# Performance work log

Hardware: AMD Instinct MI355X
Metric: run time of the kernel (lower is better)

Reference implementation:

```python
import jax, jax.numpy as jnp
import numpy as np

D_IN = 2048
D_OUT = 2048
SEQ = 4096


def setup_inputs() -> dict:
    key = jax.random.key(0)
    kx, kq, kk, kv = jax.random.split(key, 4)
    x = jax.random.normal(kx, (SEQ, D_IN), dtype=jnp.float32)
    # torch.nn.Linear weights have shape [d_out, d_in]
    s = 1.0 / np.sqrt(D_IN)
    W_q = jax.random.uniform(kq, (D_OUT, D_IN), jnp.float32, -s, s)
    W_k = jax.random.uniform(kk, (D_OUT, D_IN), jnp.float32, -s, s)
    W_v = jax.random.uniform(kv, (D_OUT, D_IN), jnp.float32, -s, s)
    return {"x": x, "W_q": W_q, "W_k": W_k, "W_v": W_v}


def reference(x, W_q, W_k, W_v):
    # projections (torch Linear: x @ W.T)
    q = x @ W_q.T  # [S, D]
    k = x @ W_k.T
    v = x @ W_v.T
    scores = q @ k.T  # [S, S]
    scale = jnp.asarray(k.shape[-1], scores.dtype) ** 0.5
    attn = jax.nn.softmax(scores / scale, axis=-1)
    # post-softmax causal mask + row renormalization (faithful to source)
    S = scores.shape[0]
    mask = jnp.tril(jnp.ones((S, S), dtype=attn.dtype))
    masked = attn * mask
    masked = masked / masked.sum(axis=1, keepdims=True)
    return masked @ v  # [S, D]
```

## Files before the change

kernel.cpp:

```cpp
#include <hip/hip_runtime.h>
#include <hip/hip_bf16.h>
#include <math.h>


typedef __attribute__((ext_vector_type(8))) short bf16x8;
typedef __attribute__((ext_vector_type(4))) float f32x4;
typedef __attribute__((ext_vector_type(8))) unsigned short u16x8;
typedef __attribute__((ext_vector_type(4))) int iv4;

__device__ __forceinline__ unsigned short f2bf(float f) {
  unsigned int u = __float_as_uint(f);
  u += 0x7FFFu + ((u >> 16) & 1u);
  return (unsigned short)(u >> 16);
}

__device__ __forceinline__ void gload16(const unsigned short* g, unsigned short* l) {
  __builtin_amdgcn_global_load_lds(
      (const __attribute__((address_space(1))) void*)g,
      (__attribute__((address_space(3))) void*)l,
      16, 0, 0);
}

template <int OFF>
__device__ __forceinline__ bf16x8 dsr(unsigned addr) {
  iv4 r;
  asm volatile("ds_read_b128 %0, %1 offset:%2" : "=v"(r) : "v"(addr), "i"(OFF));
  return __builtin_bit_cast(bf16x8, r);
}

__global__ void cvt_f32_bf16(const float* __restrict__ in,
                             unsigned short* __restrict__ out, int n) {
  int i = (blockIdx.x * 256 + threadIdx.x) * 8;
  if (i >= n) return;
  float4 a = *(const float4*)(in + i);
  float4 b = *(const float4*)(in + i + 4);
  u16x8 r;
  r[0] = f2bf(a.x); r[1] = f2bf(a.y); r[2] = f2bf(a.z); r[3] = f2bf(a.w);
  r[4] = f2bf(b.x); r[5] = f2bf(b.y); r[6] = f2bf(b.z); r[7] = f2bf(b.w);
  *(u16x8*)(out + i) = r;
}

#define LGKM_SB()                                         \
  asm volatile("s_waitcnt lgkmcnt(0)" ::: "memory");      \
  __builtin_amdgcn_sched_barrier(0)

#define QMFMA(MB, NB, AF, BV)                                                 \
  _Pragma("unroll")                                                           \
  for (int _fm = 0; _fm < 4; ++_fm)                                           \
    _Pragma("unroll")                                                         \
    for (int _fn = 0; _fn < 2; ++_fn)                                         \
      _Pragma("unroll")                                                       \
      for (int _ks = 0; _ks < 2; ++_ks)                                       \
        acc[(MB) + _fm][(NB) + _fn] = __builtin_amdgcn_mfma_f32_16x16x32_bf16( \
            AF[_fm * 2 + _ks], BV[_fn * 2 + _ks], acc[(MB) + _fm][(NB) + _fn], \
            0, 0, 0);

#define STG_A(mhv, tau, bufv)                                                 \
  do {                                                                        \
    unsigned short* _d = lds + (bufv) * 32768 + (mhv) * 8192 + w * 512;       \
    gload16(pA + (size_t)((mhv) * 64) * KC + ((size_t)(tau) << 6), _d);       \
    gload16(pA + (size_t)(128 + (mhv) * 64) * KC + ((size_t)(tau) << 6),      \
            _d + 4096);                                                       \
  } while (0)

#define STG_B(nhv, tau, bufv)                                                 \
  do {                                                                        \
    unsigned short* _d = lds + (bufv) * 32768 + 16384 + (nhv) * 8192 + w * 512;\
    gload16(pB + (size_t)((nhv) * 32) * KC + ((size_t)(tau) << 6), _d);       \
    gload16(pB + (size_t)(128 + (nhv) * 32) * KC + ((size_t)(tau) << 6),      \
            _d + 4096);                                                       \
  } while (0)

#define VM_WAIT()                                                             \
  do {                                                                        \
    if (tail) { asm volatile("s_waitcnt vmcnt(0)" ::: "memory"); }            \
    else      { asm volatile("s_waitcnt vmcnt(8)" ::: "memory"); }            \
  } while (0)

template <int KC>
__device__ __forceinline__ void gemm_core(const unsigned short* __restrict__ Ab,
                                          const unsigned short* __restrict__ Bb,
                                          unsigned short* lds, int ktiles,
                                          f32x4 (&acc)[8][4]) {
  const int tid  = threadIdx.x;
  const int lane = tid & 63;
  const int w    = tid >> 6;
  const int wm   = w >> 2;
  const int wn   = w & 3;

  const int base  = w * 8 + (lane >> 3);
  const int gslot = (lane & 7) ^ ((lane >> 3) & 7);
  const unsigned short* pA = Ab + (size_t)base * KC + gslot * 8;
  const unsigned short* pB =
      Bb + (size_t)((base >> 5) * 64 + (base & 31)) * KC + gslot * 8;

  const unsigned lb = (unsigned)(size_t)&lds[0];
  const int rl = lane & 15, g = lane >> 4;
  const unsigned sw0 = (unsigned)(((0 + g) ^ (rl & 7)) * 16);
  const unsigned sw1 = (unsigned)(((4 + g) ^ (rl & 7)) * 16);
  const unsigned rA = lb + (unsigned)(wm * 8192 + rl * 128);
  const unsigned rB = lb + (unsigned)(wn * 4096 + rl * 128);

#pragma unroll
  for (int m = 0; m < 8; ++m)
#pragma unroll
    for (int n = 0; n < 4; ++n) acc[m][n] = f32x4{0.f, 0.f, 0.f, 0.f};

  STG_A(0, 0, 0); STG_B(0, 0, 0); STG_A(1, 0, 0); STG_B(1, 0, 0);
  if (ktiles > 1) {
    STG_A(0, 1, 1); STG_B(0, 1, 1); STG_A(1, 1, 1);
    asm volatile("s_waitcnt vmcnt(6)" ::: "memory");
  } else {
    asm volatile("s_waitcnt vmcnt(0)" ::: "memory");
  }
  __builtin_amdgcn_s_barrier();

  bf16x8 af0[8], af1[8], bv0[4], bv1[4];
  {
    const unsigned aA0 = rA + sw0, aA1 = rA + sw1;
    const unsigned aB0 = rB + sw0, aB1 = rB + sw1;
    af0[0] = dsr<0>(aA0);     af0[1] = dsr<0>(aA1);
    af0[2] = dsr<2048>(aA0);  af0[3] = dsr<2048>(aA1);
    af0[4] = dsr<4096>(aA0);  af0[5] = dsr<4096>(aA1);
    af0[6] = dsr<6144>(aA0);  af0[7] = dsr<6144>(aA1);
    bv0[0] = dsr<32768>(aB0); bv0[1] = dsr<32768>(aB1);
    bv0[2] = dsr<34816>(aB0); bv0[3] = dsr<34816>(aB1);
  }

  for (int t = 0; t < ktiles; ++t) {
    const unsigned bo  = (unsigned)(t & 1) << 16;
    const unsigned bon = (unsigned)((t + 1) & 1) << 16;
    const int buf = t & 1, nb = (t + 1) & 1;
    const bool s1 = (t + 1) < ktiles, s2 = (t + 2) < ktiles;
    const bool tail = t >= ktiles - 2;
    const unsigned aA0 = rA + bo + sw0, aA1 = rA + bo + sw1;
    const unsigned aB0 = rB + bo + sw0, aB1 = rB + bo + sw1;
    const unsigned nA0 = rA + bon + sw0, nA1 = rA + bon + sw1;
    const unsigned nB0 = rB + bon + sw0, nB1 = rB + bon + sw1;

    LGKM_SB();
    af1[0] = dsr<16384>(aA0); af1[1] = dsr<16384>(aA1);
    af1[2] = dsr<18432>(aA0); af1[3] = dsr<18432>(aA1);
    af1[4] = dsr<20480>(aA0); af1[5] = dsr<20480>(aA1);
    af1[6] = dsr<22528>(aA0); af1[7] = dsr<22528>(aA1);
    __builtin_amdgcn_sched_barrier(0);
    __builtin_amdgcn_s_setprio(1);
    QMFMA(0, 0, af0, bv0);
    __builtin_amdgcn_s_setprio(0);
    if (s1) STG_B(1, t + 1, nb);
    VM_WAIT();
    __builtin_amdgcn_s_barrier();

    LGKM_SB();
    bv1[0] = dsr<49152>(aB0); bv1[1] = dsr<49152>(aB1);
    bv1[2] = dsr<51200>(aB0); bv1[3] = dsr<51200>(aB1);
    __builtin_amdgcn_sched_barrier(0);
    __builtin_amdgcn_s_setprio(1);
    QMFMA(4, 0, af1, bv0);
    __builtin_amdgcn_s_setprio(0);
    if (s2) { STG_A(0, t + 2, buf); STG_B(0, t + 2, buf); }
    VM_WAIT();
    __builtin_amdgcn_s_barrier();

    LGKM_SB();
    if (s1) {
      bv0[0] = dsr<32768>(nB0); bv0[1] = dsr<32768>(nB1);
      bv0[2] = dsr<34816>(nB0); bv0[3] = dsr<34816>(nB1);
    }
    __builtin_amdgcn_sched_barrier(0);
    __builtin_amdgcn_s_setprio(1);
    QMFMA(0, 2, af0, bv1);
    __builtin_amdgcn_s_setprio(0);
    if (s2) STG_A(1, t + 2, buf);
    VM_WAIT();
    __builtin_amdgcn_s_barrier();

    __builtin_amdgcn_sched_barrier(0);
    if (s1) {
      af0[0] = dsr<0>(nA0);     af0[1] = dsr<0>(nA1);
      af0[2] = dsr<2048>(nA0);  af0[3] = dsr<2048>(nA1);
      af0[4] = dsr<4096>(nA0);  af0[5] = dsr<4096>(nA1);
      af0[6] = dsr<6144>(nA0);  af0[7] = dsr<6144>(nA1);
    }
    __builtin_amdgcn_sched_barrier(0);
    __builtin_amdgcn_s_setprio(1);
    QMFMA(4, 2, af1, bv1);
    __builtin_amdgcn_s_setprio(0);
    VM_WAIT();
    __builtin_amdgcn_s_barrier();
  }
}

__device__ __forceinline__ void ep_f32(float* C, const f32x4 (&acc)[8][4],
                                       int r0, int c0, int ldc, float scale) {
  const int lane = threadIdx.x & 63, w = threadIdx.x >> 6;
  const int crow0 = r0 + (w >> 2) * 128 + ((lane >> 4) << 2);
  const int ccol0 = c0 + (w & 3) * 64 + (lane & 15);
#pragma unroll
  for (int m = 0; m < 8; ++m)
#pragma unroll
    for (int n = 0; n < 4; ++n)
#pragma unroll
      for (int j = 0; j < 4; ++j)
        C[(size_t)(crow0 + m * 16 + j) * ldc + (ccol0 + n * 16)] =
            acc[m][n][j] * scale;
}

__device__ __forceinline__ void ep_f32_at(float* C, const f32x4 (&acc)[8][4],
                                          int r0, int c0, int ldc, float scale) {
  const int lane = threadIdx.x & 63, w = threadIdx.x >> 6;
  const int crow0 = r0 + (w >> 2) * 128 + ((lane >> 4) << 2);
  const int ccol0 = c0 + (w & 3) * 64 + (lane & 15);
#pragma unroll
  for (int m = 0; m < 8; ++m)
#pragma unroll
    for (int n = 0; n < 4; ++n)
#pragma unroll
      for (int j = 0; j < 4; ++j)
        atomicAdd(&C[(size_t)(crow0 + m * 16 + j) * ldc + (ccol0 + n * 16)],
                  acc[m][n][j] * scale);
}

__device__ __forceinline__ void ep_bf16(unsigned short* C, const f32x4 (&acc)[8][4],
                                        int r0, int c0, int ldc) {
  const int lane = threadIdx.x & 63, w = threadIdx.x >> 6;
  const int crow0 = r0 + (w >> 2) * 128 + ((lane >> 4) << 2);
  const int ccol0 = c0 + (w & 3) * 64 + (lane & 15);
#pragma unroll
  for (int m = 0; m < 8; ++m)
#pragma unroll
    for (int n = 0; n < 4; ++n)
#pragma unroll
      for (int j = 0; j < 4; ++j)
        C[(size_t)(crow0 + m * 16 + j) * ldc + (ccol0 + n * 16)] =
            f2bf(acc[m][n][j]);
}

__global__ __launch_bounds__(512, 2)
void proj_qk(const unsigned short* __restrict__ xb,
             const unsigned short* __restrict__ wqb,
             const unsigned short* __restrict__ wkb,
             unsigned short* __restrict__ Q, unsigned short* __restrict__ Kb) {
  __shared__ __align__(16) unsigned short lds[65536];
  const int bid = blockIdx.x;
  const int wg = (bid & 7) * 32 + (bid >> 3);
  const int bm = wg >> 4, bnr = wg & 15;
  const unsigned short* B = (bnr < 8) ? wqb : wkb;
  unsigned short* C = (bnr < 8) ? Q : Kb;
  const int bnl = bnr & 7;
  f32x4 acc[8][4];
  gemm_core<2048>(xb + (size_t)bm * 256 * 2048, B + (size_t)bnl * 256 * 2048,
                  lds, 32, acc);
  ep_bf16(C, acc, bm * 256, bnl * 256, 2048);
}

__global__ __launch_bounds__(512, 2)
void vt_qkt(const unsigned short* __restrict__ Qp,
            const unsigned short* __restrict__ Kp,
            const unsigned short* __restrict__ wvb,
            const unsigned short* __restrict__ xb,
            float* __restrict__ sc, unsigned short* __restrict__ Vt,
            float scale) {
  __shared__ __align__(16) unsigned short lds[65536];
  const int id = blockIdx.x;
  f32x4 acc[8][4];
  if (id < 64) {
    const int p = id >> 2, c = id & 3;
    const size_t koff = (size_t)c * 8 * 64;
    gemm_core<2048>(Qp + (size_t)15 * 256 * 2048 + koff,
                    Kp + (size_t)p * 256 * 2048 + koff, lds, 8, acc);
    ep_f32_at(sc, acc, 3840, p * 256, 4096, scale);
  } else if (id < 184) {
    const int q = id - 64;
    int bm = 0;
    while ((bm + 1) * (bm + 2) / 2 <= q) ++bm;
    const int bn = q - bm * (bm + 1) / 2;
    gemm_core<2048>(Qp + (size_t)bm * 256 * 2048,
                    Kp + (size_t)bn * 256 * 2048, lds, 32, acc);
    ep_f32(sc, acc, bm * 256, bn * 256, 4096, scale);
  } else {
    const int v = id - 184, bm = v >> 4, bn = v & 15;
    gemm_core<2048>(wvb + (size_t)bm * 256 * 2048,
                    xb + (size_t)bn * 256 * 2048, lds, 32, acc);
    ep_bf16(Vt, acc, bm * 256, bn * 256, 4096);
  }
}

__global__ __launch_bounds__(512, 2)
void pv(const unsigned short* __restrict__ P,
        const unsigned short* __restrict__ Vt, float* __restrict__ out,
        float* __restrict__ aux) {
  __shared__ __align__(16) unsigned short lds[65536];
  const int id = blockIdx.x;
  const int j = id >> 1, h = id & 1;
  const int bm = j >> 3, bn = j & 7;
  const int kt = (bm + 1) * 4;
  const int k0 = h ? (kt >> 1) : 0;
  const int ktl = h ? (kt - (kt >> 1)) : (kt >> 1);
  f32x4 acc[8][4];
  gemm_core<4096>(P + (size_t)bm * 256 * 4096 + (size_t)k0 * 64,
                  Vt + (size_t)bn * 256 * 4096 + (size_t)k0 * 64, lds, ktl, acc);
  if (h) ep_f32(aux, acc, bm * 256, bn * 256, 2048, 1.0f);
  else   ep_f32(out, acc, bm * 256, bn * 256, 2048, 1.0f);
}

__global__ void add_f32(float* __restrict__ out, const float* __restrict__ aux,
                        int n) {
  int i = (blockIdx.x * 256 + threadIdx.x) * 8;
  if (i >= n) return;
  float4 a0 = *(const float4*)(out + i), a1 = *(const float4*)(out + i + 4);
  float4 b0 = *(const float4*)(aux + i), b1 = *(const float4*)(aux + i + 4);
  a0.x += b0.x; a0.y += b0.y; a0.z += b0.z; a0.w += b0.w;
  a1.x += b1.x; a1.y += b1.y; a1.z += b1.z; a1.w += b1.w;
  *(float4*)(out + i) = a0; *(float4*)(out + i + 4) = a1;
}

__global__ void softmax_causal(const float* __restrict__ Sc,
                               unsigned short* __restrict__ P, int S) {
  const int i = blockIdx.x;
  const int tid = threadIdx.x;
  const int nvalid = i + 1;
  const int pad_end = ((i >> 8) + 1) << 8;
  const float* row = Sc + (size_t)i * S;

  float v[16];
  float m = -1e30f;
#pragma unroll
  for (int it = 0; it < 16; ++it) {
    const int j = tid + it * 256;
    const float x = (j < nvalid) ? row[j] : -1e30f;
    v[it] = x;
    m = fmaxf(m, x);
  }
#pragma unroll
  for (int d = 1; d < 64; d <<= 1) m = fmaxf(m, __shfl_xor(m, d));
  __shared__ float red_m[4], red_s[4];
  const int lane = tid & 63, wv = tid >> 6;
  if (lane == 0) red_m[wv] = m;
  __syncthreads();
  m = fmaxf(fmaxf(red_m[0], red_m[1]), fmaxf(red_m[2], red_m[3]));

  float s = 0.0f;
#pragma unroll
  for (int it = 0; it < 16; ++it) {
    const int j = tid + it * 256;
    const float e = (j < nvalid) ? __expf(v[it] - m) : 0.0f;
    v[it] = e;
    s += e;
  }
#pragma unroll
  for (int d = 1; d < 64; d <<= 1) s += __shfl_xor(s, d);
  if (lane == 0) red_s[wv] = s;
  __syncthreads();
  s = red_s[0] + red_s[1] + red_s[2] + red_s[3];

  const float inv = 1.0f / s;
  unsigned short* prow = P + (size_t)i * S;
#pragma unroll
  for (int it = 0; it < 16; ++it) {
    const int j = tid + it * 256;
    if (j < pad_end) prow[j] = (j < nvalid) ? f2bf(v[it] * inv) : (unsigned short)0;
  }
}

extern "C" void kernel_launch(void* const* d_in, const int* in_sizes, int n_in,
                              void* d_out, int out_size, void* d_ws, size_t ws_size,
                              hipStream_t stream) {
  const float* x  = (const float*)d_in[0];
  const float* Wq = (const float*)d_in[1];
  const float* Wk = (const float*)d_in[2];
  const float* Wv = (const float*)d_in[3];
  float* out = (float*)d_out;

  const int S = 4096, D = 2048;
  char* ws = (char*)d_ws;
  const size_t MB = 1u << 20;
  float*          sc  = (float*)ws;
  float*          aux = (float*)ws;
  unsigned short* xb  = (unsigned short*)(ws + 64 * MB);
  unsigned short* wqb = (unsigned short*)(ws + 80 * MB);
  unsigned short* wkb = (unsigned short*)(ws + 88 * MB);
  unsigned short* wvb = (unsigned short*)(ws + 96 * MB);
  unsigned short* Q   = (unsigned short*)(ws + 104 * MB);
  unsigned short* Kb  = (unsigned short*)(ws + 120 * MB);
  unsigned short* Vt  = (unsigned short*)(ws + 80 * MB);
  unsigned short* P   = (unsigned short*)(ws + 104 * MB);

  cvt_f32_bf16<<<(S * D) / (256 * 8), 256, 0, stream>>>(x, xb, S * D);
  cvt_f32_bf16<<<(D * D) / (256 * 8), 256, 0, stream>>>(Wq, wqb, D * D);
  cvt_f32_bf16<<<(D * D) / (256 * 8), 256, 0, stream>>>(Wk, wkb, D * D);
  cvt_f32_bf16<<<(D * D) / (256 * 8), 256, 0, stream>>>(Wv, wvb, D * D);

  proj_qk<<<256, 512, 0, stream>>>(xb, wqb, wkb, Q, Kb);

  hipMemsetAsync(sc + (size_t)3840 * 4096, 0, (size_t)256 * 4096 * 4, stream);

  const float scale = 1.0f / sqrtf((float)D);
  vt_qkt<<<312, 512, 0, stream>>>(Q, Kb, wvb, xb, sc, Vt, scale);

  softmax_causal<<<S, 256, 0, stream>>>(sc, P, S);

  pv<<<256, 512, 0, stream>>>(P, Vt, out, aux);
  add_f32<<<(S * D) / (256 * 8), 256, 0, stream>>>(out, aux, S * D);
}
```

Baseline: 245.0 us.

## Use atomic work queues with split-K atomics for QK^T and PV

Replaces static grid decomposition in the QK^T/V^T and PV kernels with persistent blocks that pull tile ids from an atomic counter. Larger causal rows are split along K, with results accumulated by atomic adds, which removes the separate add kernel and the auxiliary buffer. The four conversion launches are merged into one kernel. The aim is better load balance over the triangular workload and fewer launches, at the cost of memsets on output and score regions, atomic contention, and nondeterministic float summation order.

```diff
diff --git a/kernel.cpp b/kernel.cpp
--- a/kernel.cpp
+++ b/kernel.cpp
@@ -28,16 +28,25 @@
   return __builtin_bit_cast(bf16x8, r);
 }
 
-__global__ void cvt_f32_bf16(const float* __restrict__ in,
-                             unsigned short* __restrict__ out, int n) {
+__global__ void cvt_all(const float* __restrict__ x, const float* __restrict__ wq,
+                        const float* __restrict__ wk, const float* __restrict__ wv,
+                        unsigned short* __restrict__ xb, unsigned short* __restrict__ wqb,
+                        unsigned short* __restrict__ wkb, unsigned short* __restrict__ wvb) {
+  const int SD = 4096 * 2048, DD = 2048 * 2048;
   int i = (blockIdx.x * 256 + threadIdx.x) * 8;
-  if (i >= n) return;
-  float4 a = *(const float4*)(in + i);
-  float4 b = *(const float4*)(in + i + 4);
+  const float* in;
+  unsigned short* out;
+  int off;
+  if (i < SD)               { in = x;  out = xb;  off = i; }
+  else if (i < SD + DD)     { in = wq; out = wqb; off = i - SD; }
+  else if (i < SD + 2 * DD) { in = wk; out = wkb; off = i - SD - DD; }
+  else                      { in = wv; out = wvb; off = i - SD - 2 * DD; }
+  float4 a = *(const float4*)(in + off);
+  float4 b = *(const float4*)(in + off + 4);
   u16x8 r;
   r[0] = f2bf(a.x); r[1] = f2bf(a.y); r[2] = f2bf(a.z); r[3] = f2bf(a.w);
   r[4] = f2bf(b.x); r[5] = f2bf(b.y); r[6] = f2bf(b.z); r[7] = f2bf(b.w);
-  *(u16x8*)(out + i) = r;
+  *(u16x8*)(out + off) = r;
 }
 
 #define LGKM_SB()                                         \
@@ -255,64 +264,76 @@
 }
 
 __global__ __launch_bounds__(512, 2)
-void vt_qkt(const unsigned short* __restrict__ Qp,
-            const unsigned short* __restrict__ Kp,
-            const unsigned short* __restrict__ wvb,
-            const unsigned short* __restrict__ xb,
-            float* __restrict__ sc, unsigned short* __restrict__ Vt,
-            float scale) {
+void vt_qkt_q(const unsigned short* __restrict__ Qp,
+              const unsigned short* __restrict__ Kp,
+              const unsigned short* __restrict__ wvb,
+              const unsigned short* __restrict__ xb,
+              float* __restrict__ sc, unsigned short* __restrict__ Vt,
+              float scale, int* __restrict__ ctr) {
   __shared__ __align__(16) unsigned short lds[65536];
-  const int id = blockIdx.x;
+  __shared__ int sid;
   f32x4 acc[8][4];
-  if (id < 64) {
-    const int p = id >> 2, c = id & 3;
-    const size_t koff = (size_t)c * 8 * 64;
-    gemm_core<2048>(Qp + (size_t)15 * 256 * 2048 + koff,
-                    Kp + (size_t)p * 256 * 2048 + koff, lds, 8, acc);
-    ep_f32_at(sc, acc, 3840, p * 256, 4096, scale);
-  } else if (id < 184) {
-    const int q = id - 64;
-    int bm = 0;
-    while ((bm + 1) * (bm + 2) / 2 <= q) ++bm;
-    const int bn = q - bm * (bm + 1) / 2;
-    gemm_core<2048>(Qp + (size_t)bm * 256 * 2048,
-                    Kp + (size_t)bn * 256 * 2048, lds, 32, acc);
-    ep_f32(sc, acc, bm * 256, bn * 256, 4096, scale);
-  } else {
-    const int v = id - 184, bm = v >> 4, bn = v & 15;
-    gemm_core<2048>(wvb + (size_t)bm * 256 * 2048,
-                    xb + (size_t)bn * 256 * 2048, lds, 32, acc);
-    ep_bf16(Vt, acc, bm * 256, bn * 256, 4096);
+  for (;;) {
+    if (threadIdx.x == 0) sid = atomicAdd(ctr, 1);
+    __syncthreads();
+    const int id = sid;
+    if (id >= 438) return;
+    if (id < 78) {
+      int bm = 0;
+      while ((bm + 1) * (bm + 2) / 2 <= id) ++bm;
+      const int bn = id - bm * (bm + 1) / 2;
+      gemm_core<2048>(Qp + (size_t)bm * 256 * 2048,
+                      Kp + (size_t)bn * 256 * 2048, lds, 32, acc);
+      ep_f32(sc, acc, bm * 256, bn * 256, 4096, scale);
+    } else if (id < 206) {
+      const int v = id - 78, bm = v >> 4, bn = v & 15;
+      gemm_core<2048>(wvb + (size_t)bm * 256 * 2048,
+                      xb + (size_t)bn * 256 * 2048, lds, 32, acc);
+      ep_bf16(Vt, acc, bm * 256, bn * 256, 4096);
+    } else {
+      const int c = id - 206, tc = c >> 2, ck = c & 3;
+      int bm, bn;
+      if (tc < 13)      { bm = 12; bn = tc; }
+      else if (tc < 27) { bm = 13; bn = tc - 13; }
+      else if (tc < 42) { bm = 14; bn = tc - 27; }
+      else              { bm = 15; bn = tc - 42; }
+      const size_t koff = (size_t)ck * 512;
+      gemm_core<2048>(Qp + (size_t)bm * 256 * 2048 + koff,
+                      Kp + (size_t)bn * 256 * 2048 + koff, lds, 8, acc);
+      ep_f32_at(sc, acc, bm * 256, bn * 256, 4096, scale);
+    }
   }
 }
 
 __global__ __launch_bounds__(512, 2)
-void pv(const unsigned short* __restrict__ P,
-        const unsigned short* __restrict__ Vt, float* __restrict__ out,
-        float* __restrict__ aux) {
+void pv_q(const unsigned short* __restrict__ P,
+          const unsigned short* __restrict__ Vt, float* __restrict__ out,
+          int* __restrict__ ctr) {
   __shared__ __align__(16) unsigned short lds[65536];
-  const int id = blockIdx.x;
-  const int j = id >> 1, h = id & 1;
-  const int bm = j >> 3, bn = j & 7;
-  const int kt = (bm + 1) * 4;
-  const int k0 = h ? (kt >> 1) : 0;
-  const int ktl = h ? (kt - (kt >> 1)) : (kt >> 1);
+  __shared__ int sid;
   f32x4 acc[8][4];
-  gemm_core<4096>(P + (size_t)bm * 256 * 4096 + (size_t)k0 * 64,
-                  Vt + (size_t)bn * 256 * 4096 + (size_t)k0 * 64, lds, ktl, acc);
-  if (h) ep_f32(aux, acc, bm * 256, bn * 256, 2048, 1.0f);
-  else   ep_f32(out, acc, bm * 256, bn * 256, 2048, 1.0f);
-}
-
-__global__ void add_f32(float* __restrict__ out, const float* __restrict__ aux,
-                        int n) {
-  int i = (blockIdx.x * 256 + threadIdx.x) * 8;
-  if (i >= n) return;
-  float4 a0 = *(const float4*)(out + i), a1 = *(const float4*)(out + i + 4);
-  float4 b0 = *(const float4*)(aux + i), b1 = *(const float4*)(aux + i + 4);
-  a0.x += b0.x; a0.y += b0.y; a0.z += b0.z; a0.w += b0.w;
-  a1.x += b1.x; a1.y += b1.y; a1.z += b1.z; a1.w += b1.w;
-  *(float4*)(out + i) = a0; *(float4*)(out + i + 4) = a1;
+  for (;;) {
+    if (threadIdx.x == 0) sid = atomicAdd(ctr, 1);
+    __syncthreads();
+    const int id = sid;
+    if (id >= 320) return;
+    int rem = id, bm = 15, s = 4;
+    for (;;) {
+      s = (bm >> 2) + 1;
+      const int cnt = 8 * s;
+      if (rem < cnt) break;
+      rem -= cnt;
+      --bm;
+    }
+    const int bn = rem / s, p = rem % s;
+    const int kt = (bm + 1) * 4;
+    const int k0 = (kt * p) / s, k1 = (kt * (p + 1)) / s;
+    gemm_core<4096>(P + (size_t)bm * 256 * 4096 + (size_t)k0 * 64,
+                    Vt + (size_t)bn * 256 * 4096 + (size_t)k0 * 64,
+                    lds, k1 - k0, acc);
+    if (s == 1) ep_f32(out, acc, bm * 256, bn * 256, 2048, 1.0f);
+    else        ep_f32_at(out, acc, bm * 256, bn * 256, 2048, 1.0f);
+  }
 }
 
 __global__ void softmax_causal(const float* __restrict__ Sc,
@@ -376,7 +397,6 @@
   char* ws = (char*)d_ws;
   const size_t MB = 1u << 20;
   float*          sc  = (float*)ws;
-  float*          aux = (float*)ws;
   unsigned short* xb  = (unsigned short*)(ws + 64 * MB);
   unsigned short* wqb = (unsigned short*)(ws + 80 * MB);
   unsigned short* wkb = (unsigned short*)(ws + 88 * MB);
@@ -385,21 +405,22 @@
   unsigned short* Kb  = (unsigned short*)(ws + 120 * MB);
   unsigned short* Vt  = (unsigned short*)(ws + 80 * MB);
   unsigned short* P   = (unsigned short*)(ws + 104 * MB);
-
-  cvt_f32_bf16<<<(S * D) / (256 * 8), 256, 0, stream>>>(x, xb, S * D);
-  cvt_f32_bf16<<<(D * D) / (256 * 8), 256, 0, stream>>>(Wq, wqb, D * D);
-  cvt_f32_bf16<<<(D * D) / (256 * 8), 256, 0, stream>>>(Wk, wkb, D * D);
-  cvt_f32_bf16<<<(D * D) / (256 * 8), 256, 0, stream>>>(Wv, wvb, D * D);
+  int*            ctr = (int*)(ws + 136 * MB);
+
+  cvt_all<<<(S * D + 3 * D * D) / (256 * 8), 256, 0, stream>>>(
+      x, Wq, Wk, Wv, xb, wqb, wkb, wvb);
+
+  hipMemsetAsync(ctr, 0, 16, stream);
+  hipMemsetAsync(sc + (size_t)3072 * 4096, 0, (size_t)1024 * 4096 * 4, stream);
 
   proj_qk<<<256, 512, 0, stream>>>(xb, wqb, wkb, Q, Kb);
 
-  hipMemsetAsync(sc + (size_t)3840 * 4096, 0, (size_t)256 * 4096 * 4, stream);
-
   const float scale = 1.0f / sqrtf((float)D);
-  vt_qkt<<<312, 512, 0, stream>>>(Q, Kb, wvb, xb, sc, Vt, scale);
+  vt_qkt_q<<<256, 512, 0, stream>>>(Q, Kb, wvb, xb, sc, Vt, scale, ctr);
 
   softmax_causal<<<S, 256, 0, stream>>>(sc, P, S);
 
-  pv<<<256, 512, 0, stream>>>(P, Vt, out, aux);
-  add_f32<<<(S * D) / (256 * 8), 256, 0, stream>>>(out, aux, S * D);
-}
+  hipMemsetAsync(out + (size_t)1024 * 2048, 0, (size_t)3072 * 2048 * 4, stream);
+
+  pv_q<<<256, 512, 0, stream>>>(P, Vt, out, ctr + 1);
+}
```

Result: slower. 300.1 us (+22.5%).
